# Kernel optimization log

Hardware: AMD Instinct MI355X
Metric: run time of the kernel (lower is better)

## Reference

```python
import jax, jax.numpy as jnp
import numpy as np

N_CHEM = 200000
N_DIS = 200000
D = 256
L = 2  # num_layers
R = 4  # relations: 0=cause(chem->dis),1=relate(chem->dis),2=rev_relate(dis->chem),3=child(dis->dis)
E = 500000


def setup_inputs() -> dict:
    key = jax.random.key(0)
    ks = jax.random.split(key, 12)
    x_chem = jax.random.normal(ks[0], (N_CHEM, D), dtype=jnp.float32)
    x_dis = jax.random.normal(ks[1], (N_DIS, D), dtype=jnp.float32)
    ei_cause = jax.random.randint(ks[2], (2, E), 0, N_CHEM, dtype=jnp.int32)
    ei_relate = jax.random.randint(ks[3], (2, E), 0, N_CHEM, dtype=jnp.int32)
    ei_rev = jax.random.randint(ks[4], (2, E), 0, N_DIS, dtype=jnp.int32)
    ei_child = jax.random.randint(ks[5], (2, E), 0, N_DIS, dtype=jnp.int32)
    scale = 1.0 / np.sqrt(D)
    # PyG SAGEConv params per (layer, relation): lin_l (W+b, applied to mean-aggregated
    # neighbors) and lin_r (W only, applied to destination/root features).
    Wl = jax.random.normal(ks[6], (L, R, D, D), dtype=jnp.float32) * scale
    bl = jnp.zeros((L, R, D), dtype=jnp.float32)
    Wr = jax.random.normal(ks[7], (L, R, D, D), dtype=jnp.float32) * scale
    return {"x_chem": x_chem, "x_dis": x_dis, "Wl": Wl, "bl": bl, "Wr": Wr,
            "ei_cause": ei_cause, "ei_relate": ei_relate, "ei_rev": ei_rev,
            "ei_child": ei_child}


def _sage(x_src, x_dst, ei, Wl, bl, Wr, n_dst):
    # SAGEConv: lin_l(mean_{j in N(i)} x_j) + lin_r(x_i)
    src, dst = ei[0], ei[1]
    msg = jnp.take(x_src, src, axis=0)                      # [E, D] gather
    s = jax.ops.segment_sum(msg, dst, num_segments=n_dst)   # [n_dst, D]
    cnt = jax.ops.segment_sum(jnp.ones((ei.shape[1],), x_src.dtype), dst,
                              num_segments=n_dst)
    mean = s / jnp.maximum(cnt, 1.0)[:, None]               # zero-degree -> 0
    return mean @ Wl + bl + x_dst @ Wr


def _hetero_layer(x_chem, x_dis, Wl, bl, Wr, ei_cause, ei_relate, ei_rev, ei_child):
    # HeteroConv(aggr='sum'): sum conv outputs per destination node type.
    out_dis = (_sage(x_chem, x_dis, ei_cause, Wl[0], bl[0], Wr[0], N_DIS)
               + _sage(x_chem, x_dis, ei_relate, Wl[1], bl[1], Wr[1], N_DIS)
               + _sage(x_dis, x_dis, ei_child, Wl[3], bl[3], Wr[3], N_DIS))
    out_chem = _sage(x_dis, x_chem, ei_rev, Wl[2], bl[2], Wr[2], N_CHEM)
    return out_chem, out_dis


def reference(x_chem, x_dis, Wl, bl, Wr, ei_cause, ei_relate, ei_rev, ei_child):
    # layers[:-1]: conv -> relu -> dropout(p=0, identity)
    for l in range(L - 1):
        x_chem, x_dis = _hetero_layer(x_chem, x_dis, Wl[l], bl[l], Wr[l],
                                      ei_cause, ei_relate, ei_rev, ei_child)
        x_chem = jax.nn.relu(x_chem)
        x_dis = jax.nn.relu(x_dis)
    # last layer: conv only
    x_chem, x_dis = _hetero_layer(x_chem, x_dis, Wl[L - 1], bl[L - 1], Wr[L - 1],
                                  ei_cause, ei_relate, ei_rev, ei_child)
    return x_chem, x_dis
```

## Files before the change

kernel.cpp:

```cpp
#include <hip/hip_runtime.h>

#define D_FEAT 256
constexpr int N_CHEM = 200000;
constexpr int N_DIS  = 200000;
constexpr int N_EDGE = 500000;
constexpr int NROWS  = 200000;
constexpr int NPAD   = 200064;
constexpr int NCNT   = 4 * NROWS;
constexpr int NEALL  = 4 * N_EDGE;

constexpr int PB_CNT = (NEALL + 255) / 256;
constexpr int PB_CVT = NROWS * D_FEAT / 4 / 256;
constexpr int PB_WT  = 1538;

typedef _Float16 f16x8 __attribute__((ext_vector_type(8)));
typedef _Float16 f16x4 __attribute__((ext_vector_type(4)));
typedef float    f32x4 __attribute__((ext_vector_type(4)));

__device__ __forceinline__ void gload_lds16(const void* g, void* l) {
    __builtin_amdgcn_global_load_lds(
        (const __attribute__((address_space(1))) void*)g,
        (__attribute__((address_space(3))) void*)l, 16, 0, 0);
}

__global__ __launch_bounds__(256) void prep_k(
    const int* __restrict__ e0, const int* __restrict__ e1,
    const int* __restrict__ e2, const int* __restrict__ e3,
    int* __restrict__ cnt,
    const float* __restrict__ x_chem, _Float16* __restrict__ xb_chem,
    const float* __restrict__ x_dis,  _Float16* __restrict__ xb_dis,
    const float* __restrict__ Wl, const float* __restrict__ Wr,
    const float* __restrict__ bl,
    _Float16* __restrict__ WT_dis, _Float16* __restrict__ WT_chem,
    float* __restrict__ bsum) {
    const int b = blockIdx.x;
    if (b < PB_CNT) {
        const int g = b * 256 + threadIdx.x;
        if (g >= NEALL) return;
        const int r = g / N_EDGE;
        const int le = g - r * N_EDGE;
        const int* e = (r == 0) ? e0 : (r == 1) ? e1 : (r == 2) ? e2 : e3;
        atomicAdd(&cnt[r * NROWS + e[N_EDGE + le]], 1);
    } else if (b < PB_CNT + 2 * PB_CVT) {
        const int b1 = b - PB_CNT;
        const float* in = (b1 < PB_CVT) ? x_chem : x_dis;
        _Float16* out = (b1 < PB_CVT) ? xb_chem : xb_dis;
        const int i = (b1 % PB_CVT) * 256 + threadIdx.x;
        const float4 v = reinterpret_cast<const float4*>(in)[i];
        f16x4 o;
        o[0] = (_Float16)v.x; o[1] = (_Float16)v.y;
        o[2] = (_Float16)v.z; o[3] = (_Float16)v.w;
        reinterpret_cast<f16x4*>(out)[i] = o;
    } else {
        const int b2 = b - PB_CNT - 2 * PB_CVT;
        const int l = b2 / PB_WT;
        const int idx = (b2 % PB_WT) * 256 + threadIdx.x;
        const float* Wl_l = Wl + (size_t)l * 4 * 65536;
        const float* Wr_l = Wr + (size_t)l * 4 * 65536;
        if (idx < 262144) {
            const int n = idx >> 10, k = idx & 1023, seg = k >> 8, kk = k & 255;
            float v;
            if (seg == 0)
                v = Wr_l[kk * 256 + n] + Wr_l[65536 + kk * 256 + n] + Wr_l[3 * 65536 + kk * 256 + n];
            else if (seg == 1) v = Wl_l[kk * 256 + n];
            else if (seg == 2) v = Wl_l[65536 + kk * 256 + n];
            else               v = Wl_l[3 * 65536 + kk * 256 + n];
            WT_dis[(size_t)l * 262144 + idx] = (_Float16)v;
        } else if (idx < 393216) {
            const int li = idx - 262144;
            const int n = li >> 9, k = li & 511, seg = k >> 8, kk = k & 255;
            const float v = (seg == 0) ? Wr_l[2 * 65536 + kk * 256 + n]
                                       : Wl_l[2 * 65536 + kk * 256 + n];
            WT_chem[(size_t)l * 131072 + li] = (_Float16)v;
        } else if (idx < 393216 + 256) {
            const int n = idx - 393216;
            const float* bb = bl + (size_t)l * 1024;
            bsum[l * 256 + n] = bb[n] + bb[256 + n] + bb[3 * 256 + n];
        }
    }
}

__global__ __launch_bounds__(256) void scan1_k(const int* __restrict__ cnt,
                                               int* __restrict__ offs,
                                               int* __restrict__ cursor,
                                               int* __restrict__ bsums, int n) {
    __shared__ int s[256];
    const int t = threadIdx.x;
    const int i = blockIdx.x * 256 + t;
    const int v = (i < n) ? cnt[i] : 0;
    s[t] = v;
    __syncthreads();
#pragma unroll
    for (int d = 1; d < 256; d <<= 1) {
        const int x = (t >= d) ? s[t - d] : 0;
        __syncthreads();
        s[t] += x;
        __syncthreads();
    }
    if (i < n) {
        const int o = s[t] - v;
        offs[i] = o;
        cursor[i] = o;
    }
    if (t == 255) bsums[blockIdx.x] = s[255];
}

__global__ __launch_bounds__(1024) void scan2_k(int* __restrict__ bsums, int nb) {
    __shared__ int s[1024];
    const int t = threadIdx.x;
    int v[4];
    int sum = 0;
#pragma unroll
    for (int q = 0; q < 4; ++q) {
        const int i = t * 4 + q;
        v[q] = (i < nb) ? bsums[i] : 0;
        sum += v[q];
    }
    s[t] = sum;
    __syncthreads();
#pragma unroll
    for (int d = 1; d < 1024; d <<= 1) {
        const int x = (t >= d) ? s[t - d] : 0;
        __syncthreads();
        s[t] += x;
        __syncthreads();
    }
    int base = s[t] - sum;
#pragma unroll
    for (int q = 0; q < 4; ++q) {
        const int i = t * 4 + q;
        if (i < nb) {
            const int tmp = v[q];
            bsums[i] = base;
            base += tmp;
        }
    }
}

__global__ __launch_bounds__(256) void fill_all_k(
    const int* __restrict__ e0, const int* __restrict__ e1,
    const int* __restrict__ e2, const int* __restrict__ e3,
    int* __restrict__ cursor, const int* __restrict__ bsums,
    int* __restrict__ csr) {
    const int g = blockIdx.x * 256 + threadIdx.x;
    if (g >= NEALL) return;
    const int r = g / N_EDGE;
    const int le = g - r * N_EDGE;
    const int* e = (r == 0) ? e0 : (r == 1) ? e1 : (r == 2) ? e2 : e3;
    const int d = r * NROWS + e[N_EDGE + le];
    const int p = atomicAdd(&cursor[d], 1) + bsums[d >> 8];
    csr[p] = e[le];
}

__global__ __launch_bounds__(256) void gather_all_k(
    const _Float16* __restrict__ srcA, const _Float16* __restrict__ srcB,
    const int* __restrict__ csr, const int* __restrict__ offs,
    const int* __restrict__ bsums, const int* __restrict__ cnt,
    _Float16* __restrict__ chunkbuf, int crp, int base, int rows) {
    const int y = blockIdx.y;
    const int rel = (y == 0) ? 0 : (y == 1) ? 1 : (y == 2) ? 3 : 2;
    const _Float16* x = (y < 2) ? srcA : srcB;
    _Float16* agg = chunkbuf + (size_t)y * crp * D_FEAT;

    const int wid = threadIdx.x >> 6;
    const int lane = threadIdx.x & 63;
    const int grp = lane >> 4;
    const int li  = lane & 15;
    const int lrow = blockIdx.x * 16 + wid * 4 + grp;
    if (lrow >= rows) return;
    const int g = rel * NROWS + base + lrow;
    const int start = offs[g] + bsums[g >> 8];
    const int n = cnt[g];
    float a0[8] = {0,0,0,0,0,0,0,0}, a1[8] = {0,0,0,0,0,0,0,0};
    const _Float16* xb = x + li * 16;
    for (int j = 0; j < n; j += 4) {
        const int rem = n - j;
        const int i0 = start + j;
        const int c1 = (rem > 1) ? 1 : 0;
        const int c2 = (rem > 2) ? 2 : 0;
        const int c3 = (rem > 3) ? 3 : 0;
        const int s0 = csr[i0];
        const int s1 = csr[i0 + c1];
        const int s2 = csr[i0 + c2];
        const int s3 = csr[i0 + c3];
        const float w1 = c1 ? 1.f : 0.f;
        const float w2 = c2 ? 1.f : 0.f;
        const float w3 = c3 ? 1.f : 0.f;
        const f16x8 u0a = *reinterpret_cast<const f16x8*>(xb + (size_t)s0 * D_FEAT);
        const f16x8 u0b = *reinterpret_cast<const f16x8*>(xb + (size_t)s0 * D_FEAT + 8);
        const f16x8 u1a = *reinterpret_cast<const f16x8*>(xb + (size_t)s1 * D_FEAT);
        const f16x8 u1b = *reinterpret_cast<const f16x8*>(xb + (size_t)s1 * D_FEAT + 8);
        const f16x8 u2a = *reinterpret_cast<const f16x8*>(xb + (size_t)s2 * D_FEAT);
        const f16x8 u2b = *reinterpret_cast<const f16x8*>(xb + (size_t)s2 * D_FEAT + 8);
        const f16x8 u3a = *reinterpret_cast<const f16x8*>(xb + (size_t)s3 * D_FEAT);
        const f16x8 u3b = *reinterpret_cast<const f16x8*>(xb + (size_t)s3 * D_FEAT + 8);
#pragma unroll
        for (int q = 0; q < 8; ++q) {
            a0[q] += (float)u0a[q];
            a0[q] = fmaf(w1, (float)u1a[q], a0[q]);
            a0[q] = fmaf(w2, (float)u2a[q], a0[q]);
            a0[q] = fmaf(w3, (float)u3a[q], a0[q]);
            a1[q] += (float)u0b[q];
            a1[q] = fmaf(w1, (float)u1b[q], a1[q]);
            a1[q] = fmaf(w2, (float)u2b[q], a1[q]);
            a1[q] = fmaf(w3, (float)u3b[q], a1[q]);
        }
    }
    const float inv = 1.0f / fmaxf((float)n, 1.0f);
    f16x8 o0, o1;
#pragma unroll
    for (int q = 0; q < 8; ++q) {
        o0[q] = (_Float16)(a0[q] * inv);
        o1[q] = (_Float16)(a1[q] * inv);
    }
    _Float16* ap = agg + (size_t)lrow * D_FEAT + li * 16;
    *reinterpret_cast<f16x8*>(ap) = o0;
    *reinterpret_cast<f16x8*>(ap + 8) = o1;
}

template <int NSEG, bool RELU_OUT>
__device__ __forceinline__ void gemm_body(
    _Float16* __restrict__ AslBase, _Float16* __restrict__ BslBase,
    const _Float16* __restrict__ A0, const _Float16* __restrict__ A1,
    const _Float16* __restrict__ A2, const _Float16* __restrict__ A3,
    const _Float16* __restrict__ WT, const float* __restrict__ bias,
    float* __restrict__ Cf, _Float16* __restrict__ Ch, int vrows) {
    constexpr int KT = NSEG * 256;
    constexpr int NS = KT / 64;
    const int t = threadIdx.x;
    const int w = t >> 6, l = t & 63;
    const int wm = w & 1, wn = w >> 1;
    const int fr = l & 15, ko = (l >> 4) << 3;
    const int row0 = blockIdx.x * 128;
    const int col0 = blockIdx.y * 128;

    f32x4 acc[4][4];
#pragma unroll
    for (int m = 0; m < 4; ++m)
#pragma unroll
        for (int n = 0; n < 4; ++n) acc[m][n] = f32x4{0.f, 0.f, 0.f, 0.f};

    const int srow = t >> 3;
    const int schk = t & 7;
    const int gchk = schk ^ (srow & 7);
    const int rsw  = (fr & 7) << 3;

    auto STAGE = [&](int buf, int ks) {
        const int seg = ks >> 2;
        const _Float16* Ab = (seg == 0) ? A0 : ((seg == 1) ? A1 : ((seg == 2) ? A2 : A3));
        const int kofs = ((ks & 3) << 6) + gchk * 8;
        _Float16* asl = AslBase + buf * 8192;
        _Float16* bsl = BslBase + buf * 8192;
#pragma unroll
        for (int is = 0; is < 4; ++is) {
            gload_lds16(Ab + (size_t)(row0 + is * 32 + srow) * D_FEAT + kofs,
                        asl + is * 2048 + w * 512);
            gload_lds16(WT + (size_t)(col0 + is * 32 + srow) * KT + seg * 256 + kofs,
                        bsl + is * 2048 + w * 512);
        }
    };

    auto COMPUTE = [&](int buf) {
        const _Float16* asl = AslBase + buf * 8192;
        const _Float16* bsl = BslBase + buf * 8192;
#pragma unroll
        for (int kk = 0; kk < 64; kk += 32) {
            f16x8 af[4], bf[4];
            const int ksw = (kk + ko) ^ rsw;
#pragma unroll
            for (int m = 0; m < 4; ++m)
                af[m] = *reinterpret_cast<const f16x8*>(&asl[(wm * 64 + m * 16 + fr) * 64 + ksw]);
#pragma unroll
            for (int n = 0; n < 4; ++n)
                bf[n] = *reinterpret_cast<const f16x8*>(&bsl[(wn * 64 + n * 16 + fr) * 64 + ksw]);
#pragma unroll
            for (int m = 0; m < 4; ++m)
#pragma unroll
                for (int n = 0; n < 4; ++n)
                    acc[m][n] = __builtin_amdgcn_mfma_f32_16x16x32_f16(af[m], bf[n], acc[m][n], 0, 0, 0);
        }
    };

    STAGE(0, 0);
    int cur = 0;
    for (int ks = 0; ks < NS - 1; ++ks) {
        STAGE(cur ^ 1, ks + 1);
        asm volatile("s_waitcnt vmcnt(8)" ::: "memory");
        __builtin_amdgcn_s_barrier();
        __builtin_amdgcn_sched_barrier(0);
        COMPUTE(cur);
        __builtin_amdgcn_sched_barrier(0);
        __builtin_amdgcn_s_barrier();
        __builtin_amdgcn_sched_barrier(0);
        cur ^= 1;
    }
    asm volatile("s_waitcnt vmcnt(0)" ::: "memory");
    __builtin_amdgcn_s_barrier();
    __builtin_amdgcn_sched_barrier(0);
    COMPUTE(cur);

    const int cro = (l >> 4) << 2;
#pragma unroll
    for (int n = 0; n < 4; ++n) {
        const int col = col0 + wn * 64 + n * 16 + fr;
        const float bi = bias[col];
#pragma unroll
        for (int m = 0; m < 4; ++m) {
            const int rbase = row0 + wm * 64 + m * 16 + cro;
#pragma unroll
            for (int j = 0; j < 4; ++j) {
                const int r = rbase + j;
                if (r < vrows) {
                    const float v = acc[m][n][j] + bi;
                    if constexpr (RELU_OUT)
                        Ch[(size_t)r * D_FEAT + col] = (_Float16)fmaxf(v, 0.f);
                    else
                        Cf[(size_t)r * D_FEAT + col] = v;
                }
            }
        }
    }
}

template <bool RELU_OUT>
__global__ __launch_bounds__(256) void gemm2_k(
    const _Float16* __restrict__ A0d, const _Float16* __restrict__ A1,
    const _Float16* __restrict__ A2, const _Float16* __restrict__ A3,
    const _Float16* __restrict__ WTd, const float* __restrict__ biasd,
    float* __restrict__ Cfd, _Float16* __restrict__ Chd,
    const _Float16* __restrict__ A0c, const _Float16* __restrict__ A4,
    const _Float16* __restrict__ WTc, const float* __restrict__ biasc,
    float* __restrict__ Cfc, _Float16* __restrict__ Chc, int vrows) {
    __shared__ _Float16 Asl[2 * 128 * 64];
    __shared__ _Float16 Bsl[2 * 128 * 64];
    if (blockIdx.z == 0)
        gemm_body<4, RELU_OUT>(Asl, Bsl, A0d, A1, A2, A3, WTd, biasd, Cfd, Chd, vrows);
    else
        gemm_body<2, RELU_OUT>(Asl, Bsl, A0c, A4, nullptr, nullptr, WTc, biasc, Cfc, Chc, vrows);
}

extern "C" void kernel_launch(void* const* d_in, const int* in_sizes, int n_in,
                              void* d_out, int out_size, void* d_ws, size_t ws_size,
                              hipStream_t stream) {
    const float* x_chem = (const float*)d_in[0];
    const float* x_dis  = (const float*)d_in[1];
    const float* Wl     = (const float*)d_in[2];
    const float* bl     = (const float*)d_in[3];
    const float* Wr     = (const float*)d_in[4];
    const int* ei[4] = {(const int*)d_in[5],
                        (const int*)d_in[6],
                        (const int*)d_in[7],
                        (const int*)d_in[8]};

    float* out_chem = (float*)d_out;
    float* out_dis  = out_chem + (size_t)N_CHEM * D_FEAT;

    constexpr size_t FB = (size_t)NPAD * D_FEAT * 2;
    char* w = (char*)d_ws;
    _Float16* h_chem  = (_Float16*)(w);
    _Float16* h_dis   = (_Float16*)(w + FB);
    _Float16* xb_chem = (_Float16*)(w + 2 * FB);
    _Float16* xb_dis  = (_Float16*)(w + 3 * FB);
    char* p = w + 4 * FB;
    int* csr    = (int*)(p);              p += 8000000;
    int* counts = (int*)(p);              p += 3200000;
    int* offs   = (int*)(p);              p += 3200000;
    int* cursor = (int*)(p);              p += 3200000;
    int* bsums  = (int*)(p);              p += 16384;
    _Float16* WT_dis  = (_Float16*)(p);   p += 1048576;
    _Float16* WT_chem = (_Float16*)(p);   p += 524288;
    float* bsum = (float*)(p);            p += 2048;
    _Float16* chunkbuf = (_Float16*)(p);

    const size_t FIXED = (size_t)(p - w);
    long long avail = (long long)ws_size - (long long)FIXED;
    int crp = 51200;
    if (avail < (long long)crp * 2048) {
        long long c = avail / 2048;
        if (c > NPAD) c = NPAD;
        crp = (int)(c & ~127LL);
        if (crp < 128) crp = 128;
    }

    const int eall_grid = (NEALL + 255) / 256;
    const int scan_blocks = (NCNT + 255) / 256;
    hipMemsetAsync(counts, 0, NCNT * sizeof(int), stream);
    prep_k<<<PB_CNT + 2 * PB_CVT + 2 * PB_WT, 256, 0, stream>>>(
        ei[0], ei[1], ei[2], ei[3], counts,
        x_chem, xb_chem, x_dis, xb_dis, Wl, Wr, bl, WT_dis, WT_chem, bsum);
    scan1_k<<<scan_blocks, 256, 0, stream>>>(counts, offs, cursor, bsums, NCNT);
    scan2_k<<<1, 1024, 0, stream>>>(bsums, scan_blocks);
    fill_all_k<<<eall_grid, 256, 0, stream>>>(ei[0], ei[1], ei[2], ei[3], cursor, bsums, csr);

    _Float16* slot0 = chunkbuf;
    _Float16* slot1 = chunkbuf + (size_t)1 * crp * D_FEAT;
    _Float16* slot2 = chunkbuf + (size_t)2 * crp * D_FEAT;
    _Float16* slot3 = chunkbuf + (size_t)3 * crp * D_FEAT;

    for (int base = 0; base < NROWS; base += crp) {
        const int rows = (NROWS - base < crp) ? (NROWS - base) : crp;
        const int rows_pad = (rows + 127) & ~127;
        const dim3 ggrid((rows + 15) / 16, 4);
        const dim3 mgrid(rows_pad / 128, 2, 2);
        gather_all_k<<<ggrid, 256, 0, stream>>>(xb_chem, xb_dis, csr, offs, bsums,
                                                counts, chunkbuf, crp, base, rows);
        gemm2_k<true><<<mgrid, 256, 0, stream>>>(
            xb_dis + (size_t)base * D_FEAT, slot0, slot1, slot2,
            WT_dis, bsum, nullptr, h_dis + (size_t)base * D_FEAT,
            xb_chem + (size_t)base * D_FEAT, slot3,
            WT_chem, bl + 2 * 256, nullptr, h_chem + (size_t)base * D_FEAT, rows);
    }

    for (int base = 0; base < NROWS; base += crp) {
        const int rows = (NROWS - base < crp) ? (NROWS - base) : crp;
        const int rows_pad = (rows + 127) & ~127;
        const dim3 ggrid((rows + 15) / 16, 4);
        const dim3 mgrid(rows_pad / 128, 2, 2);
        gather_all_k<<<ggrid, 256, 0, stream>>>(h_chem, h_dis, csr, offs, bsums,
                                                counts, chunkbuf, crp, base, rows);
        gemm2_k<false><<<mgrid, 256, 0, stream>>>(
            h_dis + (size_t)base * D_FEAT, slot0, slot1, slot2,
            WT_dis + 262144, bsum + 256, out_dis + (size_t)base * D_FEAT, nullptr,
            h_chem + (size_t)base * D_FEAT, slot3,
            WT_chem + 131072, bl + 6 * 256, out_chem + (size_t)base * D_FEAT, nullptr, rows);
    }
}
```

Baseline: 1.587 ms.

## Overlap next chunk's gather with current chunk's GEMM in a fused kernel

Introduces a fused kernel whose blocks are interleaved: every ninth block runs a GEMM tile for the current row chunk while the rest gather and mean-aggregate neighbor features for the next chunk into a second, double-buffered chunk buffer. This is meant to overlap the memory-bound gather with the compute-bound GEMM and remove the serialization between the two kernel launches per chunk. The cost is double the chunk-buffer workspace, which may shrink chunk size when workspace is limited. It also adds more complex block indexing, and the two workloads compete for CUs and LDS inside one launch.

```diff
diff --git a/kernel.cpp b/kernel.cpp
--- a/kernel.cpp
+++ b/kernel.cpp
@@ -152,21 +152,20 @@
     csr[p] = e[le];
 }
 
-__global__ __launch_bounds__(256) void gather_all_k(
+__device__ __forceinline__ void gather_body(
     const _Float16* __restrict__ srcA, const _Float16* __restrict__ srcB,
     const int* __restrict__ csr, const int* __restrict__ offs,
     const int* __restrict__ bsums, const int* __restrict__ cnt,
-    _Float16* __restrict__ chunkbuf, int crp, int base, int rows) {
-    const int y = blockIdx.y;
-    const int rel = (y == 0) ? 0 : (y == 1) ? 1 : (y == 2) ? 3 : 2;
-    const _Float16* x = (y < 2) ? srcA : srcB;
-    _Float16* agg = chunkbuf + (size_t)y * crp * D_FEAT;
+    _Float16* __restrict__ gbuf, int crp, int base, int rows, int gx, int gy) {
+    const int rel = (gy == 0) ? 0 : (gy == 1) ? 1 : (gy == 2) ? 3 : 2;
+    const _Float16* x = (gy < 2) ? srcA : srcB;
+    _Float16* agg = gbuf + (size_t)gy * crp * D_FEAT;
 
     const int wid = threadIdx.x >> 6;
     const int lane = threadIdx.x & 63;
     const int grp = lane >> 4;
     const int li  = lane & 15;
-    const int lrow = blockIdx.x * 16 + wid * 4 + grp;
+    const int lrow = gx * 16 + wid * 4 + grp;
     if (lrow >= rows) return;
     const int g = rel * NROWS + base + lrow;
     const int start = offs[g] + bsums[g >> 8];
@@ -218,21 +217,29 @@
     *reinterpret_cast<f16x8*>(ap + 8) = o1;
 }
 
+__global__ __launch_bounds__(256) void gather_all_k(
+    const _Float16* __restrict__ srcA, const _Float16* __restrict__ srcB,
+    const int* __restrict__ csr, const int* __restrict__ offs,
+    const int* __restrict__ bsums, const int* __restrict__ cnt,
+    _Float16* __restrict__ gbuf, int crp, int base, int rows) {
+    gather_body(srcA, srcB, csr, offs, bsums, cnt, gbuf, crp, base, rows,
+                blockIdx.x, blockIdx.y);
+}
+
 template <int NSEG, bool RELU_OUT>
 __device__ __forceinline__ void gemm_body(
     _Float16* __restrict__ AslBase, _Float16* __restrict__ BslBase,
     const _Float16* __restrict__ A0, const _Float16* __restrict__ A1,
     const _Float16* __restrict__ A2, const _Float16* __restrict__ A3,
     const _Float16* __restrict__ WT, const float* __restrict__ bias,
-    float* __restrict__ Cf, _Float16* __restrict__ Ch, int vrows) {
+    float* __restrict__ Cf, _Float16* __restrict__ Ch, int vrows,
+    int row0, int col0) {
     constexpr int KT = NSEG * 256;
     constexpr int NS = KT / 64;
     const int t = threadIdx.x;
     const int w = t >> 6, l = t & 63;
     const int wm = w & 1, wn = w >> 1;
     const int fr = l & 15, ko = (l >> 4) << 3;
-    const int row0 = blockIdx.x * 128;
-    const int col0 = blockIdx.y * 128;
 
     f32x4 acc[4][4];
 #pragma unroll
@@ -333,10 +340,48 @@
     float* __restrict__ Cfc, _Float16* __restrict__ Chc, int vrows) {
     __shared__ _Float16 Asl[2 * 128 * 64];
     __shared__ _Float16 Bsl[2 * 128 * 64];
+    const int row0 = blockIdx.x * 128, col0 = blockIdx.y * 128;
     if (blockIdx.z == 0)
-        gemm_body<4, RELU_OUT>(Asl, Bsl, A0d, A1, A2, A3, WTd, biasd, Cfd, Chd, vrows);
+        gemm_body<4, RELU_OUT>(Asl, Bsl, A0d, A1, A2, A3, WTd, biasd, Cfd, Chd, vrows, row0, col0);
     else
-        gemm_body<2, RELU_OUT>(Asl, Bsl, A0c, A4, nullptr, nullptr, WTc, biasc, Cfc, Chc, vrows);
+        gemm_body<2, RELU_OUT>(Asl, Bsl, A0c, A4, nullptr, nullptr, WTc, biasc, Cfc, Chc, vrows, row0, col0);
+}
+
+template <bool RELU_OUT>
+__global__ __launch_bounds__(256) void fused_k(
+    const _Float16* __restrict__ A0d, const _Float16* __restrict__ A1,
+    const _Float16* __restrict__ A2, const _Float16* __restrict__ A3,
+    const _Float16* __restrict__ WTd, const float* __restrict__ biasd,
+    float* __restrict__ Cfd, _Float16* __restrict__ Chd,
+    const _Float16* __restrict__ A0c, const _Float16* __restrict__ A4,
+    const _Float16* __restrict__ WTc, const float* __restrict__ biasc,
+    float* __restrict__ Cfc, _Float16* __restrict__ Chc,
+    int vrows, int gemmBX, int G,
+    const _Float16* __restrict__ srcA, const _Float16* __restrict__ srcB,
+    const int* __restrict__ csr, const int* __restrict__ offs,
+    const int* __restrict__ bsums, const int* __restrict__ cnt,
+    _Float16* __restrict__ gbuf, int crp, int gbase, int grows,
+    int gxExt, int H) {
+    __shared__ _Float16 Asl[2 * 128 * 64];
+    __shared__ _Float16 Bsl[2 * 128 * 64];
+    const int b = blockIdx.x;
+    if ((b % 9) == 0 && (b / 9) < G) {
+        const int gi = b / 9;
+        const int x = gi % gemmBX;
+        const int yz = gi / gemmBX;
+        const int row0 = x * 128, col0 = (yz & 1) * 128;
+        if ((yz >> 1) == 0)
+            gemm_body<4, RELU_OUT>(Asl, Bsl, A0d, A1, A2, A3, WTd, biasd, Cfd, Chd, vrows, row0, col0);
+        else
+            gemm_body<2, RELU_OUT>(Asl, Bsl, A0c, A4, nullptr, nullptr, WTc, biasc, Cfc, Chc, vrows, row0, col0);
+    } else {
+        int ng = (b + 8) / 9;
+        if (ng > G) ng = G;
+        const int gi = b - ng;
+        if (gi >= H) return;
+        gather_body(srcA, srcB, csr, offs, bsums, cnt, gbuf, crp, gbase, grows,
+                    gi % gxExt, gi / gxExt);
+    }
 }
 
 extern "C" void kernel_launch(void* const* d_in, const int* in_sizes, int n_in,
@@ -375,12 +420,14 @@
     const size_t FIXED = (size_t)(p - w);
     long long avail = (long long)ws_size - (long long)FIXED;
     int crp = 51200;
-    if (avail < (long long)crp * 2048) {
-        long long c = avail / 2048;
+    if (avail < (long long)crp * 4096) {
+        long long c = avail / 4096;
         if (c > NPAD) c = NPAD;
         crp = (int)(c & ~127LL);
         if (crp < 128) crp = 128;
     }
+    const int nc = (NROWS + crp - 1) / crp;
+    const size_t setStride = (size_t)4 * crp * D_FEAT;
 
     const int eall_grid = (NEALL + 255) / 256;
     const int scan_blocks = (NCNT + 255) / 256;
@@ -392,36 +439,83 @@
     scan2_k<<<1, 1024, 0, stream>>>(bsums, scan_blocks);
     fill_all_k<<<eall_grid, 256, 0, stream>>>(ei[0], ei[1], ei[2], ei[3], cursor, bsums, csr);
 
-    _Float16* slot0 = chunkbuf;
-    _Float16* slot1 = chunkbuf + (size_t)1 * crp * D_FEAT;
-    _Float16* slot2 = chunkbuf + (size_t)2 * crp * D_FEAT;
-    _Float16* slot3 = chunkbuf + (size_t)3 * crp * D_FEAT;
-
-    for (int base = 0; base < NROWS; base += crp) {
-        const int rows = (NROWS - base < crp) ? (NROWS - base) : crp;
-        const int rows_pad = (rows + 127) & ~127;
-        const dim3 ggrid((rows + 15) / 16, 4);
-        const dim3 mgrid(rows_pad / 128, 2, 2);
-        gather_all_k<<<ggrid, 256, 0, stream>>>(xb_chem, xb_dis, csr, offs, bsums,
-                                                counts, chunkbuf, crp, base, rows);
-        gemm2_k<true><<<mgrid, 256, 0, stream>>>(
-            xb_dis + (size_t)base * D_FEAT, slot0, slot1, slot2,
-            WT_dis, bsum, nullptr, h_dis + (size_t)base * D_FEAT,
-            xb_chem + (size_t)base * D_FEAT, slot3,
-            WT_chem, bl + 2 * 256, nullptr, h_chem + (size_t)base * D_FEAT, rows);
-    }
-
-    for (int base = 0; base < NROWS; base += crp) {
-        const int rows = (NROWS - base < crp) ? (NROWS - base) : crp;
-        const int rows_pad = (rows + 127) & ~127;
-        const dim3 ggrid((rows + 15) / 16, 4);
-        const dim3 mgrid(rows_pad / 128, 2, 2);
-        gather_all_k<<<ggrid, 256, 0, stream>>>(h_chem, h_dis, csr, offs, bsums,
-                                                counts, chunkbuf, crp, base, rows);
-        gemm2_k<false><<<mgrid, 256, 0, stream>>>(
-            h_dis + (size_t)base * D_FEAT, slot0, slot1, slot2,
-            WT_dis + 262144, bsum + 256, out_dis + (size_t)base * D_FEAT, nullptr,
-            h_chem + (size_t)base * D_FEAT, slot3,
-            WT_chem + 131072, bl + 6 * 256, out_chem + (size_t)base * D_FEAT, nullptr, rows);
-    }
-}
+    for (int layer = 0; layer < 2; ++layer) {
+        const _Float16* srcA = layer ? h_chem : xb_chem;
+        const _Float16* srcB = layer ? h_dis  : xb_dis;
+        const _Float16* WTd = WT_dis + (size_t)layer * 262144;
+        const _Float16* WTc = WT_chem + (size_t)layer * 131072;
+        const float* biasd = bsum + layer * 256;
+        const float* biasc = bl + (layer * 4 + 2) * 256;
+
+        auto launch_gemm_ptrs = [&](int i, const _Float16*& A0d, const _Float16*& A0c,
+                                    float*& Cfd, _Float16*& Chd, float*& Cfc,
+                                    _Float16*& Chc, _Float16*& set) {
+            const size_t boff = (size_t)i * crp * D_FEAT;
+            A0d = srcB + boff;
+            A0c = srcA + boff;
+            set = chunkbuf + (size_t)(i & 1) * setStride;
+            if (layer == 0) {
+                Cfd = nullptr; Chd = h_dis + boff;
+                Cfc = nullptr; Chc = h_chem + boff;
+            } else {
+                Cfd = out_dis + boff;  Chd = nullptr;
+                Cfc = out_chem + boff; Chc = nullptr;
+            }
+        };
+
+        {
+            const int rows0 = (NROWS < crp) ? NROWS : crp;
+            gather_all_k<<<dim3((rows0 + 15) / 16, 4), 256, 0, stream>>>(
+                srcA, srcB, csr, offs, bsums, counts, chunkbuf, crp, 0, rows0);
+        }
+        for (int i = 0; i + 1 < nc; ++i) {
+            const int base_i = i * crp;
+            const int rows_i = (NROWS - base_i < crp) ? (NROWS - base_i) : crp;
+            const int base_n = (i + 1) * crp;
+            const int rows_n = (NROWS - base_n < crp) ? (NROWS - base_n) : crp;
+            const int BX = ((rows_i + 127) & ~127) / 128;
+            const int G = BX * 4;
+            const int gxExt = (rows_n + 15) / 16;
+            const int H = gxExt * 4;
+            int T = 9 * G - 8;
+            if (G + H > T) T = G + H;
+            const _Float16 *A0d, *A0c; float *Cfd, *Cfc; _Float16 *Chd, *Chc, *set;
+            launch_gemm_ptrs(i, A0d, A0c, Cfd, Chd, Cfc, Chc, set);
+            _Float16* gset = chunkbuf + (size_t)((i + 1) & 1) * setStride;
+            if (layer == 0)
+                fused_k<true><<<T, 256, 0, stream>>>(
+                    A0d, set, set + crp * D_FEAT, set + 2 * (size_t)crp * D_FEAT,
+                    WTd, biasd, Cfd, Chd,
+                    A0c, set + 3 * (size_t)crp * D_FEAT, WTc, biasc, Cfc, Chc,
+                    rows_i, BX, G,
+                    srcA, srcB, csr, offs, bsums, counts, gset, crp, base_n, rows_n,
+                    gxExt, H);
+            else
+                fused_k<false><<<T, 256, 0, stream>>>(
+                    A0d, set, set + crp * D_FEAT, set + 2 * (size_t)crp * D_FEAT,
+                    WTd, biasd, Cfd, Chd,
+                    A0c, set + 3 * (size_t)crp * D_FEAT, WTc, biasc, Cfc, Chc,
+                    rows_i, BX, G,
+                    srcA, srcB, csr, offs, bsums, counts, gset, crp, base_n, rows_n,
+                    gxExt, H);
+        }
+        {
+            const int i = nc - 1;
+            const int base_i = i * crp;
+            const int rows_i = NROWS - base_i;
+            const int BX = ((rows_i + 127) & ~127) / 128;
+            const _Float16 *A0d, *A0c; float *Cfd, *Cfc; _Float16 *Chd, *Chc, *set;
+            launch_gemm_ptrs(i, A0d, A0c, Cfd, Chd, Cfc, Chc, set);
+            if (layer == 0)
+                gemm2_k<true><<<dim3(BX, 2, 2), 256, 0, stream>>>(
+                    A0d, set, set + crp * D_FEAT, set + 2 * (size_t)crp * D_FEAT,
+                    WTd, biasd, Cfd, Chd,
+                    A0c, set + 3 * (size_t)crp * D_FEAT, WTc, biasc, Cfc, Chc, rows_i);
+            else
+                gemm2_k<false><<<dim3(BX, 2, 2), 256, 0, stream>>>(
+                    A0d, set, set + crp * D_FEAT, set + 2 * (size_t)crp * D_FEAT,
+                    WTd, biasd, Cfd, Chd,
+                    A0c, set + 3 * (size_t)crp * D_FEAT, WTc, biasc, Cfc, Chc, rows_i);
+        }
+    }
+}
```

Result: slower. 1.895 ms (+19.4%).

## Widen GEMM tile to full 256 output columns with 512-thread blocks

Applied to the files above, without the earlier changes.

The fused GEMM now has each block compute a 128x256 tile, covering all output columns, with 8 waves arranged 2x4, in place of two 128x128 column blocks. Each A row-tile is loaded from global memory once rather than twice. The B stage buffer is doubled, which raises LDS use to 96KB per block and may lower occupancy. The host loops are folded into a per-layer loop with the same semantics.

```diff
diff --git a/kernel.cpp b/kernel.cpp
--- a/kernel.cpp
+++ b/kernel.cpp
@@ -220,19 +220,17 @@
 
 template <int NSEG, bool RELU_OUT>
 __device__ __forceinline__ void gemm_body(
-    _Float16* __restrict__ AslBase, _Float16* __restrict__ BslBase,
+    _Float16* __restrict__ Asl, _Float16* __restrict__ Bsl,
     const _Float16* __restrict__ A0, const _Float16* __restrict__ A1,
     const _Float16* __restrict__ A2, const _Float16* __restrict__ A3,
     const _Float16* __restrict__ WT, const float* __restrict__ bias,
-    float* __restrict__ Cf, _Float16* __restrict__ Ch, int vrows) {
+    float* __restrict__ Cf, _Float16* __restrict__ Ch, int vrows, int row0) {
     constexpr int KT = NSEG * 256;
     constexpr int NS = KT / 64;
     const int t = threadIdx.x;
     const int w = t >> 6, l = t & 63;
-    const int wm = w & 1, wn = w >> 1;
+    const int wm = w >> 2, wn = w & 3;
     const int fr = l & 15, ko = (l >> 4) << 3;
-    const int row0 = blockIdx.x * 128;
-    const int col0 = blockIdx.y * 128;
 
     f32x4 acc[4][4];
 #pragma unroll
@@ -249,20 +247,21 @@
         const int seg = ks >> 2;
         const _Float16* Ab = (seg == 0) ? A0 : ((seg == 1) ? A1 : ((seg == 2) ? A2 : A3));
         const int kofs = ((ks & 3) << 6) + gchk * 8;
-        _Float16* asl = AslBase + buf * 8192;
-        _Float16* bsl = BslBase + buf * 8192;
-#pragma unroll
-        for (int is = 0; is < 4; ++is) {
-            gload_lds16(Ab + (size_t)(row0 + is * 32 + srow) * D_FEAT + kofs,
-                        asl + is * 2048 + w * 512);
-            gload_lds16(WT + (size_t)(col0 + is * 32 + srow) * KT + seg * 256 + kofs,
-                        bsl + is * 2048 + w * 512);
-        }
+        _Float16* asl = Asl + buf * 8192;
+        _Float16* bsl = Bsl + buf * 16384;
+#pragma unroll
+        for (int is = 0; is < 2; ++is)
+            gload_lds16(Ab + (size_t)(row0 + is * 64 + srow) * D_FEAT + kofs,
+                        asl + is * 4096 + w * 512);
+#pragma unroll
+        for (int is = 0; is < 4; ++is)
+            gload_lds16(WT + (size_t)(is * 64 + srow) * KT + seg * 256 + kofs,
+                        bsl + is * 4096 + w * 512);
     };
 
     auto COMPUTE = [&](int buf) {
-        const _Float16* asl = AslBase + buf * 8192;
-        const _Float16* bsl = BslBase + buf * 8192;
+        const _Float16* asl = Asl + buf * 8192;
+        const _Float16* bsl = Bsl + buf * 16384;
 #pragma unroll
         for (int kk = 0; kk < 64; kk += 32) {
             f16x8 af[4], bf[4];
@@ -285,7 +284,7 @@
     int cur = 0;
     for (int ks = 0; ks < NS - 1; ++ks) {
         STAGE(cur ^ 1, ks + 1);
-        asm volatile("s_waitcnt vmcnt(8)" ::: "memory");
+        asm volatile("s_waitcnt vmcnt(6)" ::: "memory");
         __builtin_amdgcn_s_barrier();
         __builtin_amdgcn_sched_barrier(0);
         COMPUTE(cur);
@@ -302,7 +301,7 @@
     const int cro = (l >> 4) << 2;
 #pragma unroll
     for (int n = 0; n < 4; ++n) {
-        const int col = col0 + wn * 64 + n * 16 + fr;
+        const int col = wn * 64 + n * 16 + fr;
         const float bi = bias[col];
 #pragma unroll
         for (int m = 0; m < 4; ++m) {
@@ -323,7 +322,7 @@
 }
 
 template <bool RELU_OUT>
-__global__ __launch_bounds__(256) void gemm2_k(
+__global__ __launch_bounds__(512) void gemm2_k(
     const _Float16* __restrict__ A0d, const _Float16* __restrict__ A1,
     const _Float16* __restrict__ A2, const _Float16* __restrict__ A3,
     const _Float16* __restrict__ WTd, const float* __restrict__ biasd,
@@ -332,11 +331,12 @@
     const _Float16* __restrict__ WTc, const float* __restrict__ biasc,
     float* __restrict__ Cfc, _Float16* __restrict__ Chc, int vrows) {
     __shared__ _Float16 Asl[2 * 128 * 64];
-    __shared__ _Float16 Bsl[2 * 128 * 64];
-    if (blockIdx.z == 0)
-        gemm_body<4, RELU_OUT>(Asl, Bsl, A0d, A1, A2, A3, WTd, biasd, Cfd, Chd, vrows);
+    __shared__ _Float16 Bsl[2 * 256 * 64];
+    const int row0 = blockIdx.x * 128;
+    if (blockIdx.y == 0)
+        gemm_body<4, RELU_OUT>(Asl, Bsl, A0d, A1, A2, A3, WTd, biasd, Cfd, Chd, vrows, row0);
     else
-        gemm_body<2, RELU_OUT>(Asl, Bsl, A0c, A4, nullptr, nullptr, WTc, biasc, Cfc, Chc, vrows);
+        gemm_body<2, RELU_OUT>(Asl, Bsl, A0c, A4, nullptr, nullptr, WTc, biasc, Cfc, Chc, vrows, row0);
 }
 
 extern "C" void kernel_launch(void* const* d_in, const int* in_sizes, int n_in,
@@ -381,6 +381,7 @@
         crp = (int)(c & ~127LL);
         if (crp < 128) crp = 128;
     }
+    const int nc = (NROWS + crp - 1) / crp;
 
     const int eall_grid = (NEALL + 255) / 256;
     const int scan_blocks = (NCNT + 255) / 256;
@@ -397,31 +398,35 @@
     _Float16* slot2 = chunkbuf + (size_t)2 * crp * D_FEAT;
     _Float16* slot3 = chunkbuf + (size_t)3 * crp * D_FEAT;
 
-    for (int base = 0; base < NROWS; base += crp) {
-        const int rows = (NROWS - base < crp) ? (NROWS - base) : crp;
-        const int rows_pad = (rows + 127) & ~127;
-        const dim3 ggrid((rows + 15) / 16, 4);
-        const dim3 mgrid(rows_pad / 128, 2, 2);
-        gather_all_k<<<ggrid, 256, 0, stream>>>(xb_chem, xb_dis, csr, offs, bsums,
-                                                counts, chunkbuf, crp, base, rows);
-        gemm2_k<true><<<mgrid, 256, 0, stream>>>(
-            xb_dis + (size_t)base * D_FEAT, slot0, slot1, slot2,
-            WT_dis, bsum, nullptr, h_dis + (size_t)base * D_FEAT,
-            xb_chem + (size_t)base * D_FEAT, slot3,
-            WT_chem, bl + 2 * 256, nullptr, h_chem + (size_t)base * D_FEAT, rows);
-    }
-
-    for (int base = 0; base < NROWS; base += crp) {
-        const int rows = (NROWS - base < crp) ? (NROWS - base) : crp;
-        const int rows_pad = (rows + 127) & ~127;
-        const dim3 ggrid((rows + 15) / 16, 4);
-        const dim3 mgrid(rows_pad / 128, 2, 2);
-        gather_all_k<<<ggrid, 256, 0, stream>>>(h_chem, h_dis, csr, offs, bsums,
-                                                counts, chunkbuf, crp, base, rows);
-        gemm2_k<false><<<mgrid, 256, 0, stream>>>(
-            h_dis + (size_t)base * D_FEAT, slot0, slot1, slot2,
-            WT_dis + 262144, bsum + 256, out_dis + (size_t)base * D_FEAT, nullptr,
-            h_chem + (size_t)base * D_FEAT, slot3,
-            WT_chem + 131072, bl + 6 * 256, out_chem + (size_t)base * D_FEAT, nullptr, rows);
-    }
-}
+    for (int layer = 0; layer < 2; ++layer) {
+        const _Float16* srcA = layer ? h_chem : xb_chem;
+        const _Float16* srcB = layer ? h_dis  : xb_dis;
+        const _Float16* WTd = WT_dis + (size_t)layer * 262144;
+        const _Float16* WTc = WT_chem + (size_t)layer * 131072;
+        const float* biasd = bsum + layer * 256;
+        const float* biasc = bl + (layer * 4 + 2) * 256;
+
+        for (int i = 0; i < nc; ++i) {
+            const int base = i * crp;
+            const int rows = (NROWS - base < crp) ? (NROWS - base) : crp;
+            const int rows_pad = (rows + 127) & ~127;
+            const size_t boff = (size_t)base * D_FEAT;
+            const dim3 ggrid((rows + 15) / 16, 4);
+            const dim3 mgrid(rows_pad / 128, 2);
+            gather_all_k<<<ggrid, 256, 0, stream>>>(srcA, srcB, csr, offs, bsums,
+                                                    counts, chunkbuf, crp, base, rows);
+            if (layer == 0)
+                gemm2_k<true><<<mgrid, 512, 0, stream>>>(
+                    srcB + boff, slot0, slot1, slot2, WTd, biasd,
+                    nullptr, h_dis + boff,
+                    srcA + boff, slot3, WTc, biasc,
+                    nullptr, h_chem + boff, rows);
+            else
+                gemm2_k<false><<<mgrid, 512, 0, stream>>>(
+                    srcB + boff, slot0, slot1, slot2, WTd, biasd,
+                    out_dis + boff, nullptr,
+                    srcA + boff, slot3, WTc, biasc,
+                    out_chem + boff, nullptr, rows);
+        }
+    }
+}
```

Result: slower. 1.659 ms (+4.5%).
